# Optimization experiments

Hardware: AMD Instinct MI355X
Metric: run time of the kernel (lower is better)

The kernel has to match this reference:

```python
import jax, jax.numpy as jnp
import numpy as np

H, W, DIM, NB = 64, 128, 768, 8
BS = DIM // NB
LAM = 0.01  # sparsity_threshold
EPS = 1e-5


def _layernorm(x, g, b):
    mu = jnp.mean(x, axis=-1, keepdims=True)
    var = jnp.mean(jnp.square(x - mu), axis=-1, keepdims=True)
    return (x - mu) * jax.lax.rsqrt(var + EPS) * g + b


def _softshrink(v):
    return jnp.sign(v) * jnp.maximum(jnp.abs(v) - LAM, 0.0)


def setup_inputs() -> dict:
    key = jax.random.key(0)
    ks = jax.random.split(key, 6)
    B = 4
    x = jax.random.normal(ks[0], (B, H * W, DIM), dtype=jnp.float32)
    w1 = 0.02 * jax.random.normal(ks[1], (NB, BS, BS), dtype=jnp.float32)
    b1 = 0.02 * jax.random.normal(ks[2], (NB, BS), dtype=jnp.float32)
    w2 = 0.02 * jax.random.normal(ks[3], (NB, BS, BS), dtype=jnp.float32)
    b2 = 0.02 * jax.random.normal(ks[4], (NB, BS), dtype=jnp.float32)
    km = jax.random.split(ks[5], 2)
    mlp_w1 = (1.0 / np.sqrt(DIM)) * jax.random.normal(km[0], (DIM, 4 * DIM), dtype=jnp.float32)
    mlp_w2 = (1.0 / np.sqrt(4 * DIM)) * jax.random.normal(km[1], (4 * DIM, DIM), dtype=jnp.float32)
    return {
        'x': x, 'w1': w1, 'b1': b1, 'w2': w2, 'b2': b2,
        'ln1_w': jnp.ones((DIM,), jnp.float32), 'ln1_b': jnp.zeros((DIM,), jnp.float32),
        'ln2_w': jnp.ones((DIM,), jnp.float32), 'ln2_b': jnp.zeros((DIM,), jnp.float32),
        'mlp_w1': mlp_w1, 'mlp_b1': jnp.zeros((4 * DIM,), jnp.float32),
        'mlp_w2': mlp_w2, 'mlp_b2': jnp.zeros((DIM,), jnp.float32),
    }


def reference(x, w1, b1, w2, b2, ln1_w, ln1_b, ln2_w, ln2_b, mlp_w1, mlp_b1, mlp_w2, mlp_b2):
    B = x.shape[0]
    xs = x.reshape(B, H, W, DIM)
    residual = xs
    xn = _layernorm(xs, ln1_w, ln1_b)
    xn = jnp.transpose(xn, (0, 3, 1, 2))  # [B, dim, h, w]
    xf = jnp.fft.rfft2(xn, norm='ortho')  # [B, dim, h, w//2+1] complex64
    Wf = xf.shape[-1]
    xf = xf.reshape(B, NB, BS, H, Wf)
    xr, xi = xf.real, xf.imag

    def bmm(t, Wm):  # block-diagonal matmul over feature dim j->m
        return jnp.einsum('bnjkl,njm->bnmkl', t, Wm)

    bb1 = b1[None, :, :, None, None]
    bb2 = b2[None, :, :, None, None]
    # NOTE: faithful to source -- both real and imag paths use the SAME weight matrix.
    o1r = jax.nn.relu(bmm(xr, w1) - bmm(xi, w1) + bb1)
    o1i = jax.nn.relu(bmm(xi, w1) + bmm(xr, w1) + bb1)
    o2r = bmm(o1r, w2) - bmm(o1i, w2) + bb2
    o2i = bmm(o1i, w2) + bmm(o1r, w2) + bb2
    o2 = _softshrink(o2r) + 1j * _softshrink(o2i)
    o2 = o2.reshape(B, DIM, H, Wf)
    xsp = jnp.fft.irfft2(o2, s=(H, W), norm='ortho')  # [B, dim, h, w]
    xsp = jnp.transpose(xsp, (0, 2, 3, 1)) + residual
    residual2 = xsp
    xn2 = _layernorm(xsp, ln2_w, ln2_b)
    hdd = jax.nn.gelu(xn2 @ mlp_w1 + mlp_b1, approximate=False)
    out = hdd @ mlp_w2 + mlp_b2 + residual2
    return out.reshape(B, H * W, DIM)
```

## Files before the change

kernel.cpp:

```cpp
#include <hip/hip_runtime.h>
#include <hip/hip_bf16.h>
#include <math.h>

#define B_    4
#define H_    64
#define W_    128
#define WF_   65
#define D_    768
#define NB_   8
#define BS_   96
#define HID_  3072
#define NTOK_ 32768
#define CHTOK_ 8192
#define LAM_  0.01f

typedef __hip_bfloat16 bf16;
typedef __attribute__((ext_vector_type(8))) short bf16x8;
typedef __attribute__((ext_vector_type(4))) float f32x4;
typedef unsigned int u32;

__device__ __forceinline__ float ldf(const float* p) { return *p; }
__device__ __forceinline__ float ldf(const bf16* p)  { return __bfloat162float(*p); }
__device__ __forceinline__ void stf(float* p, float v) { *p = v; }
__device__ __forceinline__ void stf(bf16* p, float v)  { *p = __float2bfloat16(v); }

#define GLOAD_LDS16(g, l) \
  __builtin_amdgcn_global_load_lds((const __attribute__((address_space(1))) u32*)(g), \
                                   (__attribute__((address_space(3))) u32*)(l), 16, 0, 0)

#define FRAG(arr, KP, row, kof) (*(const bf16x8*)((arr) + (size_t)(row) * (KP) + (kof)))

#define LUT_S1_OFF  0
#define LUT_S2M_OFF 22528
#define LUT_S2P_OFF 36864
#define LUT_S3_OFF  51200
#define LUT_TOTAL   77824

__global__ __launch_bounds__(256) void lut_init(bf16* __restrict__ lut) {
  const int idx = blockIdx.x * 256 + threadIdx.x;
  const float s1 = 0.011048543456039806f;
  float val = 0.f;
  if (idx < 22528) {
    int a = idx;
    if (a < 21760) {
      bool isC2 = a >= 10880; if (isC2) a -= 10880;
      int f = a / 136, w = a - f * 136;
      if (w < 128) {
        int p = (f * w) & 127;
        float ang = p * 0.04908738521234052f;
        val = isC2 ? -s1 * sinf(ang) : s1 * cosf(ang);
      }
    }
  } else if (idx < 51200) {
    int a = idx - 22528;
    float esign = -1.f;
    if (a >= 14336) { a -= 14336; esign = 1.f; }
    if (a < 13824) {
      int which = a / 4608; a -= which * 4608;
      int k = a / 72, h = a - k * 72;
      if (h < 64) {
        int p = (k * h) & 63;
        float ang = p * 0.09817477042468103f;
        float c = cosf(ang), s = esign * sinf(ang);
        val = (which == 0) ? c : ((which == 1) ? s : -s);
      }
    }
  } else {
    int a = idx - 51200;
    bool isCi = a >= 13312; if (isCi) a -= 13312;
    int w = a / 104, f = a - w * 104;
    if (f < WF_) {
      int p = (f * w) & 127;
      float ang = p * 0.04908738521234052f;
      float al = (f == 0 || f == 64) ? 1.0f : 2.0f;
      val = isCi ? -s1 * al * sinf(ang) : s1 * al * cosf(ang);
    }
  }
  lut[idx] = __float2bfloat16(val);
}

template <typename TIN>
__global__ __launch_bounds__(256) void ln_kernel(
    const TIN* __restrict__ x, const float* __restrict__ g,
    const float* __restrict__ bta, bf16* __restrict__ out) {
  __shared__ float sred[8];
  const size_t base = (size_t)blockIdx.x * D_;
  const int t = threadIdx.x;
  float v0 = ldf(x + base + t);
  float v1 = ldf(x + base + t + 256);
  float v2 = ldf(x + base + t + 512);
  float s = v0 + v1 + v2;
  #pragma unroll
  for (int o = 32; o; o >>= 1) s += __shfl_down(s, o, 64);
  int lane = t & 63, wid = t >> 6;
  if (lane == 0) sred[wid] = s;
  __syncthreads();
  if (t == 0) sred[0] = sred[0] + sred[1] + sred[2] + sred[3];
  __syncthreads();
  float mean = sred[0] * (1.0f / D_);
  float d0 = v0 - mean, d1 = v1 - mean, d2 = v2 - mean;
  float q = d0 * d0 + d1 * d1 + d2 * d2;
  #pragma unroll
  for (int o = 32; o; o >>= 1) q += __shfl_down(q, o, 64);
  if (lane == 0) sred[4 + wid] = q;
  __syncthreads();
  if (t == 0) sred[4] = sred[4] + sred[5] + sred[6] + sred[7];
  __syncthreads();
  float rstd = rsqrtf(sred[4] * (1.0f / D_) + 1e-5f);
  stf(out + base + t,       d0 * rstd * g[t]       + bta[t]);
  stf(out + base + t + 256, d1 * rstd * g[t + 256] + bta[t + 256]);
  stf(out + base + t + 512, d2 * rstd * g[t + 512] + bta[t + 512]);
}

__global__ __launch_bounds__(256) void s1_rfftw(
    const bf16* __restrict__ xn, const bf16* __restrict__ lut,
    bf16* __restrict__ fr, bf16* __restrict__ fi) {
  const int KP = 136;
  __shared__ __align__(16) bf16 sC[22528];
  __shared__ __align__(16) bf16 sXt[64 * 136];
  const int t = threadIdx.x;
  const int bh = blockIdx.x;
  const int c0 = blockIdx.y * 64;

  #pragma unroll
  for (int it = 0; it < 11; ++it)
    GLOAD_LDS16((const char*)lut + t * 16 + it * 4096, (char*)sC + t * 16 + it * 4096);

  {
    const int cv = (t & 7) * 8;
    #pragma unroll
    for (int rep = 0; rep < 4; ++rep) {
      int w = (t >> 3) + 32 * rep;
      bf16x8 v = *(const bf16x8*)(xn + ((size_t)bh * W_ + w) * D_ + c0 + cv);
      #pragma unroll
      for (int i = 0; i < 8; ++i) sXt[(cv + i) * KP + w] = ((const bf16*)&v)[i];
    }
  }
  __syncthreads();
  const bf16* sC1 = sC;
  const bf16* sC2 = sC + 10880;

  const int wave = t >> 6, lane = t & 63, l16 = lane & 15, quad = lane >> 4;
  const int ni = (wave == 0) ? 2 : 1;
  int itile[2] = {wave, 4};
  f32x4 accR[2][4], accI[2][4];
  #pragma unroll
  for (int ii = 0; ii < 2; ++ii)
    #pragma unroll
    for (int j = 0; j < 4; ++j) { accR[ii][j] = (f32x4){0,0,0,0}; accI[ii][j] = (f32x4){0,0,0,0}; }

  for (int s = 0; s < 4; ++s) {
    const int kof = s * 32 + quad * 8;
    bf16x8 bfrag[4];
    #pragma unroll
    for (int j = 0; j < 4; ++j) bfrag[j] = FRAG(sXt, KP, j * 16 + l16, kof);
    for (int ii = 0; ii < ni; ++ii) {
      const int arow = 16 * itile[ii] + l16;
      bf16x8 a1 = FRAG(sC1, KP, arow, kof);
      bf16x8 a2 = FRAG(sC2, KP, arow, kof);
      #pragma unroll
      for (int j = 0; j < 4; ++j) {
        accR[ii][j] = __builtin_amdgcn_mfma_f32_16x16x32_bf16(a1, bfrag[j], accR[ii][j], 0, 0, 0);
        accI[ii][j] = __builtin_amdgcn_mfma_f32_16x16x32_bf16(a2, bfrag[j], accI[ii][j], 0, 0, 0);
      }
    }
  }
  for (int ii = 0; ii < ni; ++ii) {
    #pragma unroll
    for (int r = 0; r < 4; ++r) {
      const int f = 16 * itile[ii] + quad * 4 + r;
      if (f >= WF_) continue;
      const size_t ob = ((size_t)bh * WF_ + f) * D_ + c0;
      #pragma unroll
      for (int j = 0; j < 4; ++j) {
        fr[ob + j * 16 + l16] = __float2bfloat16(accR[ii][j][r]);
        fi[ob + j * 16 + l16] = __float2bfloat16(accI[ii][j][r]);
      }
    }
  }
}

__global__ __launch_bounds__(256) void s2_ffth(
    const bf16* __restrict__ inr, const bf16* __restrict__ ini,
    bf16* __restrict__ outr, bf16* __restrict__ outi, const bf16* __restrict__ lut) {
  const int KP = 72;
  __shared__ __align__(16) bf16 sT[14336];
  __shared__ __align__(16) bf16 sFtr[64 * 72];
  __shared__ __align__(16) bf16 sFti[64 * 72];
  const int t = threadIdx.x;
  const int b = blockIdx.x / WF_;
  const int f = blockIdx.x % WF_;
  const int c0 = blockIdx.y * 64;

  #pragma unroll
  for (int it = 0; it < 7; ++it)
    GLOAD_LDS16((const char*)lut + t * 16 + it * 4096, (char*)sT + t * 16 + it * 4096);

  {
    const int cv = (t & 7) * 8;
    #pragma unroll
    for (int rep = 0; rep < 2; ++rep) {
      int h = (t >> 3) + 32 * rep;
      size_t g = ((size_t)(b * H_ + h) * WF_ + f) * D_ + c0 + cv;
      bf16x8 vr = *(const bf16x8*)(inr + g);
      bf16x8 vi = *(const bf16x8*)(ini + g);
      #pragma unroll
      for (int i = 0; i < 8; ++i) {
        sFtr[(cv + i) * KP + h] = ((const bf16*)&vr)[i];
        sFti[(cv + i) * KP + h] = ((const bf16*)&vi)[i];
      }
    }
  }
  __syncthreads();
  const bf16* sTr = sT;
  const bf16* sTi = sT + 4608;
  const bf16* sTn = sT + 9216;

  const int wave = t >> 6, lane = t & 63, l16 = lane & 15, quad = lane >> 4;
  f32x4 accR[4], accI[4];
  #pragma unroll
  for (int j = 0; j < 4; ++j) { accR[j] = (f32x4){0,0,0,0}; accI[j] = (f32x4){0,0,0,0}; }

  #pragma unroll
  for (int s = 0; s < 2; ++s) {
    const int kof = s * 32 + quad * 8;
    const int arow = 16 * wave + l16;
    bf16x8 ar = FRAG(sTr, KP, arow, kof);
    bf16x8 ai = FRAG(sTi, KP, arow, kof);
    bf16x8 an = FRAG(sTn, KP, arow, kof);
    #pragma unroll
    for (int j = 0; j < 4; ++j) {
      const int brow = j * 16 + l16;
      bf16x8 br = FRAG(sFtr, KP, brow, kof);
      bf16x8 bi = FRAG(sFti, KP, brow, kof);
      accR[j] = __builtin_amdgcn_mfma_f32_16x16x32_bf16(ar, br, accR[j], 0, 0, 0);
      accR[j] = __builtin_amdgcn_mfma_f32_16x16x32_bf16(an, bi, accR[j], 0, 0, 0);
      accI[j] = __builtin_amdgcn_mfma_f32_16x16x32_bf16(ai, br, accI[j], 0, 0, 0);
      accI[j] = __builtin_amdgcn_mfma_f32_16x16x32_bf16(ar, bi, accI[j], 0, 0, 0);
    }
  }
  #pragma unroll
  for (int r = 0; r < 4; ++r) {
    const int k = 16 * wave + quad * 4 + r;
    const size_t ob = ((size_t)(b * H_ + k) * WF_ + f) * D_ + c0;
    #pragma unroll
    for (int j = 0; j < 4; ++j) {
      outr[ob + j * 16 + l16] = __float2bfloat16(accR[j][r]);
      outi[ob + j * 16 + l16] = __float2bfloat16(accI[j][r]);
    }
  }
}

__global__ __launch_bounds__(256) void s3_irfftw(
    const bf16* __restrict__ fr, const bf16* __restrict__ fi,
    const bf16* __restrict__ lut, const float* __restrict__ x0, bf16* __restrict__ xsp) {
  const int KP = 104;
  __shared__ __align__(16) bf16 sC[26624];
  __shared__ __align__(16) bf16 sGtr[64 * 104];
  __shared__ __align__(16) bf16 sGti[64 * 104];
  const int t = threadIdx.x;
  const int bh = blockIdx.x;
  const int c0 = blockIdx.y * 64;

  #pragma unroll
  for (int it = 0; it < 13; ++it)
    GLOAD_LDS16((const char*)lut + t * 16 + it * 4096, (char*)sC + t * 16 + it * 4096);

  {
    const int cv = (t & 7) * 8;
    #pragma unroll
    for (int rep = 0; rep < 2; ++rep) {
      int f = (t >> 3) + 32 * rep;
      size_t g = ((size_t)bh * WF_ + f) * D_ + c0 + cv;
      bf16x8 vr = *(const bf16x8*)(fr + g);
      bf16x8 vi = *(const bf16x8*)(fi + g);
      #pragma unroll
      for (int i = 0; i < 8; ++i) {
        sGtr[(cv + i) * KP + f] = ((const bf16*)&vr)[i];
        sGti[(cv + i) * KP + f] = ((const bf16*)&vi)[i];
      }
    }
    if (t < 8) {
      size_t g = ((size_t)bh * WF_ + 64) * D_ + c0 + cv;
      bf16x8 vr = *(const bf16x8*)(fr + g);
      bf16x8 vi = *(const bf16x8*)(fi + g);
      #pragma unroll
      for (int i = 0; i < 8; ++i) {
        sGtr[(cv + i) * KP + 64] = ((const bf16*)&vr)[i];
        sGti[(cv + i) * KP + 64] = ((const bf16*)&vi)[i];
      }
    }
    const bf16 z = __float2bfloat16(0.f);
    for (int e = t; e < 64 * 31; e += 256) {
      int c = e / 31, f = 65 + (e - (e / 31) * 31);
      sGtr[c * KP + f] = z;
      sGti[c * KP + f] = z;
    }
  }
  __syncthreads();
  const bf16* sCr = sC;
  const bf16* sCi = sC + 13312;

  const int wave = t >> 6, lane = t & 63, l16 = lane & 15, quad = lane >> 4;
  f32x4 acc[2][4];
  #pragma unroll
  for (int ii = 0; ii < 2; ++ii)
    #pragma unroll
    for (int j = 0; j < 4; ++j) acc[ii][j] = (f32x4){0,0,0,0};

  #pragma unroll
  for (int s = 0; s < 3; ++s) {
    const int kof = s * 32 + quad * 8;
    bf16x8 br[4], bi[4];
    #pragma unroll
    for (int j = 0; j < 4; ++j) {
      br[j] = FRAG(sGtr, KP, j * 16 + l16, kof);
      bi[j] = FRAG(sGti, KP, j * 16 + l16, kof);
    }
    #pragma unroll
    for (int ii = 0; ii < 2; ++ii) {
      const int arow = 16 * (wave + 4 * ii) + l16;
      bf16x8 a1 = FRAG(sCr, KP, arow, kof);
      bf16x8 a2 = FRAG(sCi, KP, arow, kof);
      #pragma unroll
      for (int j = 0; j < 4; ++j) {
        acc[ii][j] = __builtin_amdgcn_mfma_f32_16x16x32_bf16(a1, br[j], acc[ii][j], 0, 0, 0);
        acc[ii][j] = __builtin_amdgcn_mfma_f32_16x16x32_bf16(a2, bi[j], acc[ii][j], 0, 0, 0);
      }
    }
  }
  #pragma unroll
  for (int ii = 0; ii < 2; ++ii) {
    #pragma unroll
    for (int r = 0; r < 4; ++r) {
      const int w = 16 * (wave + 4 * ii) + quad * 4 + r;
      const size_t ob = ((size_t)bh * W_ + w) * D_ + c0;
      #pragma unroll
      for (int j = 0; j < 4; ++j) {
        const size_t o = ob + j * 16 + l16;
        xsp[o] = __float2bfloat16(acc[ii][j][r] + x0[o]);
      }
    }
  }
}

__global__ __launch_bounds__(256) void blockmlp_mfma(
    bf16* __restrict__ gr, bf16* __restrict__ gi,
    const float* __restrict__ w1, const float* __restrict__ b1,
    const float* __restrict__ w2, const float* __restrict__ b2) {
  const int KP = 104;
  __shared__ __align__(16) bf16 sA[128 * 104];
  __shared__ __align__(16) bf16 sW[96 * 104];
  const int t = threadIdx.x;
  const int p0 = blockIdx.x * 64;
  const int nb = blockIdx.y;
  const int cbase = nb * BS_;

  #pragma unroll
  for (int it = 0; it < 3; ++it) {
    int task = t + 256 * it;
    int r = task / 12, jv = task - r * 12;
    size_t g = (size_t)(p0 + r) * D_ + cbase + jv * 8;
    bf16x8 vr = *(const bf16x8*)(gr + g);
    bf16x8 vi = *(const bf16x8*)(gi + g);
    bf16x8 u8, v8;
    #pragma unroll
    for (int i = 0; i < 8; ++i) {
      float xr = __bfloat162float(((const bf16*)&vr)[i]);
      float xi = __bfloat162float(((const bf16*)&vi)[i]);
      ((bf16*)&u8)[i] = __float2bfloat16(xr - xi);
      ((bf16*)&v8)[i] = __float2bfloat16(xr + xi);
    }
    *(bf16x8*)(sA + r * KP + jv * 8) = u8;
    *(bf16x8*)(sA + (64 + r) * KP + jv * 8) = v8;
  }
  {
    const float* wsrc = w1 + nb * BS_ * BS_;
    #pragma unroll
    for (int it = 0; it < 9; ++it) {
      int e4 = t + 256 * it;
      int j = e4 / 24, m4 = (e4 - j * 24) * 4;
      float4 ld = *(const float4*)(wsrc + j * 96 + m4);
      sW[(m4 + 0) * KP + j] = __float2bfloat16(ld.x);
      sW[(m4 + 1) * KP + j] = __float2bfloat16(ld.y);
      sW[(m4 + 2) * KP + j] = __float2bfloat16(ld.z);
      sW[(m4 + 3) * KP + j] = __float2bfloat16(ld.w);
    }
  }
  __syncthreads();

  const int wave = t >> 6, lane = t & 63, l16 = lane & 15, quad = lane >> 4;
  f32x4 accU[6], accV[6];
  #pragma unroll
  for (int n = 0; n < 6; ++n) { accU[n] = (f32x4){0,0,0,0}; accV[n] = (f32x4){0,0,0,0}; }

  #pragma unroll
  for (int s = 0; s < 3; ++s) {
    const int kof = s * 32 + quad * 8;
    bf16x8 au = FRAG(sA, KP, wave * 16 + l16, kof);
    bf16x8 av = FRAG(sA, KP, 64 + wave * 16 + l16, kof);
    bf16x8 bw[6];
    #pragma unroll
    for (int n = 0; n < 6; ++n) bw[n] = FRAG(sW, KP, n * 16 + l16, kof);
    #pragma unroll
    for (int n = 0; n < 6; ++n) {
      accU[n] = __builtin_amdgcn_mfma_f32_16x16x32_bf16(au, bw[n], accU[n], 0, 0, 0);
      accV[n] = __builtin_amdgcn_mfma_f32_16x16x32_bf16(av, bw[n], accV[n], 0, 0, 0);
    }
  }
  __syncthreads();

  {
    const float* wsrc = w2 + nb * BS_ * BS_;
    #pragma unroll
    for (int it = 0; it < 9; ++it) {
      int e4 = t + 256 * it;
      int j = e4 / 24, m4 = (e4 - j * 24) * 4;
      float4 ld = *(const float4*)(wsrc + j * 96 + m4);
      sW[(m4 + 0) * KP + j] = __float2bfloat16(ld.x);
      sW[(m4 + 1) * KP + j] = __float2bfloat16(ld.y);
      sW[(m4 + 2) * KP + j] = __float2bfloat16(ld.z);
      sW[(m4 + 3) * KP + j] = __float2bfloat16(ld.w);
    }
  }
  #pragma unroll
  for (int n = 0; n < 6; ++n) {
    const float bias = b1[cbase + n * 16 + l16];
    #pragma unroll
    for (int r = 0; r < 4; ++r) {
      float o1r = fmaxf(accU[n][r] + bias, 0.0f);
      float o1i = fmaxf(accV[n][r] + bias, 0.0f);
      const int row = wave * 16 + quad * 4 + r;
      sA[row * KP + n * 16 + l16]        = __float2bfloat16(o1r - o1i);
      sA[(64 + row) * KP + n * 16 + l16] = __float2bfloat16(o1r + o1i);
    }
  }
  __syncthreads();

  #pragma unroll
  for (int n = 0; n < 6; ++n) { accU[n] = (f32x4){0,0,0,0}; accV[n] = (f32x4){0,0,0,0}; }
  #pragma unroll
  for (int s = 0; s < 3; ++s) {
    const int kof = s * 32 + quad * 8;
    bf16x8 ap = FRAG(sA, KP, wave * 16 + l16, kof);
    bf16x8 aq = FRAG(sA, KP, 64 + wave * 16 + l16, kof);
    bf16x8 bw[6];
    #pragma unroll
    for (int n = 0; n < 6; ++n) bw[n] = FRAG(sW, KP, n * 16 + l16, kof);
    #pragma unroll
    for (int n = 0; n < 6; ++n) {
      accU[n] = __builtin_amdgcn_mfma_f32_16x16x32_bf16(ap, bw[n], accU[n], 0, 0, 0);
      accV[n] = __builtin_amdgcn_mfma_f32_16x16x32_bf16(aq, bw[n], accV[n], 0, 0, 0);
    }
  }

  #pragma unroll
  for (int n = 0; n < 6; ++n) {
    const float bias = b2[cbase + n * 16 + l16];
    #pragma unroll
    for (int r = 0; r < 4; ++r) {
      const int row = wave * 16 + quad * 4 + r;
      float o2r = accU[n][r] + bias;
      float o2i = accV[n][r] + bias;
      o2r = (o2r > LAM_) ? (o2r - LAM_) : ((o2r < -LAM_) ? (o2r + LAM_) : 0.0f);
      o2i = (o2i > LAM_) ? (o2i - LAM_) : ((o2i < -LAM_) ? (o2i + LAM_) : 0.0f);
      const size_t o = (size_t)(p0 + row) * D_ + cbase + n * 16 + l16;
      gr[o] = __float2bfloat16(o2r);
      gi[o] = __float2bfloat16(o2i);
    }
  }
}

__global__ __launch_bounds__(256) void wtrans_kernel(
    const float* __restrict__ Wm, bf16* __restrict__ Wt, int K, int N) {
  __shared__ float tile[32][33];
  const int n0 = blockIdx.x * 32;
  const int k0 = blockIdx.y * 32;
  const int tx = threadIdx.x & 31;
  const int ty = threadIdx.x >> 5;
  #pragma unroll
  for (int r = 0; r < 32; r += 8)
    tile[ty + r][tx] = Wm[(size_t)(k0 + ty + r) * N + n0 + tx];
  __syncthreads();
  #pragma unroll
  for (int r = 0; r < 32; r += 8)
    Wt[(size_t)(n0 + ty + r) * K + k0 + tx] = __float2bfloat16(tile[tx][ty + r]);
}

template <int MODE, typename TOUT>
__global__ __launch_bounds__(256) void mfma_gemm_kernel(
    const bf16* __restrict__ A, const bf16* __restrict__ Bt,
    const float* __restrict__ bias, const bf16* __restrict__ resid,
    TOUT* __restrict__ out, int M, int N, int K) {
  __shared__ __align__(16) bf16 As[2][128 * 32];
  __shared__ __align__(16) bf16 Bs[2][128 * 32];
  const int t = threadIdx.x;
  const int m0 = blockIdx.x * 128;
  const int n0 = blockIdx.y * 128;
  const int wave = t >> 6;
  const int lane = t & 63;
  const int wm = (wave & 1) * 64;
  const int wn = (wave >> 1) * 64;
  const int l16 = lane & 15;
  const int quad = lane >> 4;

  const int srow = t >> 2;
  const int skof = ((t & 3) ^ ((srow >> 1) & 3)) * 8;
  const bf16* Ag0 = A + (size_t)(m0 + srow) * K + skof;
  const bf16* Ag1 = A + (size_t)(m0 + 64 + srow) * K + skof;
  const bf16* Bg0 = Bt + (size_t)(n0 + srow) * K + skof;
  const bf16* Bg1 = Bt + (size_t)(n0 + 64 + srow) * K + skof;

  int aoff[4], boff[4];
  #pragma unroll
  for (int i = 0; i < 4; ++i) {
    const int ra = wm + i * 16 + l16;
    aoff[i] = ra * 32 + (quad ^ ((ra >> 1) & 3)) * 8;
    const int rb = wn + i * 16 + l16;
    boff[i] = rb * 32 + (quad ^ ((rb >> 1) & 3)) * 8;
  }

  f32x4 acc[4][4];
  #pragma unroll
  for (int i = 0; i < 4; ++i)
    #pragma unroll
    for (int j = 0; j < 4; ++j) acc[i][j] = (f32x4){0.f, 0.f, 0.f, 0.f};

#define STAGE_G(bb, ko) do { \
    GLOAD_LDS16(Ag0 + (ko), &As[bb][t * 8]); \
    GLOAD_LDS16(Ag1 + (ko), &As[bb][2048 + t * 8]); \
    GLOAD_LDS16(Bg0 + (ko), &Bs[bb][t * 8]); \
    GLOAD_LDS16(Bg1 + (ko), &Bs[bb][2048 + t * 8]); } while (0)

#define COMPUTE_T(bb) do { \
    bf16x8 af[4], bfr[4]; \
    _Pragma("unroll") \
    for (int i = 0; i < 4; ++i) af[i] = *(const bf16x8*)(As[bb] + aoff[i]); \
    _Pragma("unroll") \
    for (int j = 0; j < 4; ++j) bfr[j] = *(const bf16x8*)(Bs[bb] + boff[j]); \
    _Pragma("unroll") \
    for (int i = 0; i < 4; ++i) \
      _Pragma("unroll") \
      for (int j = 0; j < 4; ++j) \
        acc[i][j] = __builtin_amdgcn_mfma_f32_16x16x32_bf16(af[i], bfr[j], acc[i][j], 0, 0, 0); \
  } while (0)

  const int NT = K >> 5;
  STAGE_G(0, 0);
  asm volatile("s_waitcnt vmcnt(0)" ::: "memory");
  __builtin_amdgcn_s_barrier();
  asm volatile("" ::: "memory");
  int cur = 0;
  for (int tt = 0; tt + 1 < NT; ++tt) {
    STAGE_G(cur ^ 1, (tt + 1) << 5);
    COMPUTE_T(cur);
    asm volatile("s_waitcnt vmcnt(0)" ::: "memory");
    __builtin_amdgcn_s_barrier();
    asm volatile("" ::: "memory");
    cur ^= 1;
  }
  COMPUTE_T(cur);
#undef STAGE_G
#undef COMPUTE_T

  #pragma unroll
  for (int i = 0; i < 4; ++i) {
    #pragma unroll
    for (int j = 0; j < 4; ++j) {
      const int n = n0 + wn + j * 16 + l16;
      const float bz = bias[n];
      #pragma unroll
      for (int r = 0; r < 4; ++r) {
        const int m = m0 + wm + i * 16 + quad * 4 + r;
        float v = acc[i][j][r] + bz;
        if (MODE == 0) {
          float q = v * fmaf(0.044715f, v * v, 1.0f);
          float e = __expf(-1.5957691216f * q);
          v = v * __builtin_amdgcn_rcpf(1.0f + e);
        } else {
          v += ldf(resid + (size_t)m * N + n);
        }
        stf(out + (size_t)m * N + n, v);
      }
    }
  }
}

extern "C" void kernel_launch(void* const* d_in, const int* in_sizes, int n_in,
                              void* d_out, int out_size, void* d_ws, size_t ws_size,
                              hipStream_t stream) {
  const float* x     = (const float*)d_in[0];
  const float* w1    = (const float*)d_in[1];
  const float* b1    = (const float*)d_in[2];
  const float* w2    = (const float*)d_in[3];
  const float* b2    = (const float*)d_in[4];
  const float* ln1w  = (const float*)d_in[5];
  const float* ln1b  = (const float*)d_in[6];
  const float* ln2w  = (const float*)d_in[7];
  const float* ln2b  = (const float*)d_in[8];
  const float* mlpw1 = (const float*)d_in[9];
  const float* mlpb1 = (const float*)d_in[10];
  const float* mlpw2 = (const float*)d_in[11];
  const float* mlpb2 = (const float*)d_in[12];
  float* out = (float*)d_out;

  const size_t SPA = (size_t)B_ * H_ * W_ * D_;
  const size_t FRE = (size_t)B_ * H_ * WF_ * D_;
  bf16* ws   = (bf16*)d_ws;
  bf16* bufA = ws;
  bf16* Fr   = bufA + SPA;
  bf16* Fi   = Fr + FRE;
  bf16* Gr   = Fi + FRE;
  bf16* Gi   = Gr + FRE;
  bf16* hid  = Fr;
  bf16* xn2c = Gr;
  bf16* w1t  = xn2c + (size_t)CHTOK_ * D_;
  bf16* w2t  = w1t + (size_t)D_ * HID_;

  bf16* lut = (bf16*)d_out;

  const int nspec = B_ * H_ * WF_;

  hipLaunchKernelGGL(lut_init, dim3(LUT_TOTAL / 256), dim3(256), 0, stream, lut);
  hipLaunchKernelGGL((ln_kernel<float>), dim3(NTOK_), dim3(256), 0, stream, x, ln1w, ln1b, bufA);
  hipLaunchKernelGGL(s1_rfftw, dim3(B_ * H_, D_ / 64), dim3(256), 0, stream,
                     bufA, lut + LUT_S1_OFF, Fr, Fi);
  hipLaunchKernelGGL(s2_ffth, dim3(B_ * WF_, D_ / 64), dim3(256), 0, stream,
                     Fr, Fi, Gr, Gi, lut + LUT_S2M_OFF);
  hipLaunchKernelGGL(blockmlp_mfma, dim3(nspec / 64, NB_), dim3(256), 0, stream,
                     Gr, Gi, w1, b1, w2, b2);
  hipLaunchKernelGGL(s2_ffth, dim3(B_ * WF_, D_ / 64), dim3(256), 0, stream,
                     Gr, Gi, Fr, Fi, lut + LUT_S2P_OFF);
  hipLaunchKernelGGL(s3_irfftw, dim3(B_ * H_, D_ / 64), dim3(256), 0, stream,
                     Fr, Fi, lut + LUT_S3_OFF, x, bufA);

  hipLaunchKernelGGL(wtrans_kernel, dim3(HID_ / 32, D_ / 32), dim3(256), 0, stream,
                     mlpw1, w1t, D_, HID_);
  hipLaunchKernelGGL(wtrans_kernel, dim3(D_ / 32, HID_ / 32), dim3(256), 0, stream,
                     mlpw2, w2t, HID_, D_);

  for (int c = 0; c < B_; ++c) {
    const bf16* rs = bufA + (size_t)c * CHTOK_ * D_;
    float* oc = out + (size_t)c * CHTOK_ * D_;
    hipLaunchKernelGGL((ln_kernel<bf16>), dim3(CHTOK_), dim3(256), 0, stream,
                       rs, ln2w, ln2b, xn2c);
    hipLaunchKernelGGL((mfma_gemm_kernel<0, bf16>), dim3(CHTOK_ / 128, HID_ / 128), dim3(256), 0,
                       stream, xn2c, w1t, mlpb1, (const bf16*)nullptr, hid, CHTOK_, HID_, D_);
    hipLaunchKernelGGL((mfma_gemm_kernel<1, float>), dim3(CHTOK_ / 128, D_ / 128), dim3(256), 0,
                       stream, hid, w2t, mlpb2, rs, oc, CHTOK_, D_, HID_);
  }
}
```

Measured before the change: 945.3 us.

## Triple-buffer MFMA GEMM LDS staging with partial vmcnt waits and setprio

```diff
diff --git a/kernel.cpp b/kernel.cpp
--- a/kernel.cpp
+++ b/kernel.cpp
@@ -492,8 +492,8 @@
     const bf16* __restrict__ A, const bf16* __restrict__ Bt,
     const float* __restrict__ bias, const bf16* __restrict__ resid,
     TOUT* __restrict__ out, int M, int N, int K) {
-  __shared__ __align__(16) bf16 As[2][128 * 32];
-  __shared__ __align__(16) bf16 Bs[2][128 * 32];
+  __shared__ __align__(16) bf16 As[3][128 * 32];
+  __shared__ __align__(16) bf16 Bs[3][128 * 32];
   const int t = threadIdx.x;
   const int m0 = blockIdx.x * 128;
   const int n0 = blockIdx.y * 128;
@@ -538,30 +538,37 @@
     for (int i = 0; i < 4; ++i) af[i] = *(const bf16x8*)(As[bb] + aoff[i]); \
     _Pragma("unroll") \
     for (int j = 0; j < 4; ++j) bfr[j] = *(const bf16x8*)(Bs[bb] + boff[j]); \
+    __builtin_amdgcn_s_setprio(1); \
     _Pragma("unroll") \
     for (int i = 0; i < 4; ++i) \
       _Pragma("unroll") \
       for (int j = 0; j < 4; ++j) \
         acc[i][j] = __builtin_amdgcn_mfma_f32_16x16x32_bf16(af[i], bfr[j], acc[i][j], 0, 0, 0); \
+    __builtin_amdgcn_s_setprio(0); \
   } while (0)
+
+#define WAITBAR(n) do { \
+    asm volatile("s_waitcnt vmcnt(" #n ")" ::: "memory"); \
+    __builtin_amdgcn_s_barrier(); \
+    asm volatile("" ::: "memory"); } while (0)
 
   const int NT = K >> 5;
   STAGE_G(0, 0);
-  asm volatile("s_waitcnt vmcnt(0)" ::: "memory");
-  __builtin_amdgcn_s_barrier();
-  asm volatile("" ::: "memory");
-  int cur = 0;
-  for (int tt = 0; tt + 1 < NT; ++tt) {
-    STAGE_G(cur ^ 1, (tt + 1) << 5);
-    COMPUTE_T(cur);
-    asm volatile("s_waitcnt vmcnt(0)" ::: "memory");
-    __builtin_amdgcn_s_barrier();
-    asm volatile("" ::: "memory");
-    cur ^= 1;
-  }
-  COMPUTE_T(cur);
+  STAGE_G(1, 32);
+  WAITBAR(4);
+  int bcur = 0, bnxt = 1, bstg = 2;
+  for (int tt = 0; tt < NT - 2; ++tt) {
+    STAGE_G(bstg, (tt + 2) << 5);
+    COMPUTE_T(bcur);
+    WAITBAR(4);
+    int tmp = bcur; bcur = bnxt; bnxt = bstg; bstg = tmp;
+  }
+  COMPUTE_T(bcur);
+  WAITBAR(0);
+  COMPUTE_T(bnxt);
 #undef STAGE_G
 #undef COMPUTE_T
+#undef WAITBAR
 
   #pragma unroll
   for (int i = 0; i < 4; ++i) {
```

Measured after the change: 924.2 us. 2.2% less time.

## Enlarge MLP GEMM tile to 128x256 with 8 waves and triple-buffered K=64 stages

Applied to the files above, without the earlier changes.

```diff
diff --git a/kernel.cpp b/kernel.cpp
--- a/kernel.cpp
+++ b/kernel.cpp
@@ -488,37 +488,33 @@
 }
 
 template <int MODE, typename TOUT>
-__global__ __launch_bounds__(256) void mfma_gemm_kernel(
+__global__ __launch_bounds__(512) void mfma_gemm_kernel(
     const bf16* __restrict__ A, const bf16* __restrict__ Bt,
     const float* __restrict__ bias, const bf16* __restrict__ resid,
     TOUT* __restrict__ out, int M, int N, int K) {
-  __shared__ __align__(16) bf16 As[2][128 * 32];
-  __shared__ __align__(16) bf16 Bs[2][128 * 32];
+  __shared__ __align__(16) bf16 sM[3 * 24576];
   const int t = threadIdx.x;
   const int m0 = blockIdx.x * 128;
-  const int n0 = blockIdx.y * 128;
-  const int wave = t >> 6;
-  const int lane = t & 63;
-  const int wm = (wave & 1) * 64;
-  const int wn = (wave >> 1) * 64;
-  const int l16 = lane & 15;
-  const int quad = lane >> 4;
-
-  const int srow = t >> 2;
-  const int skof = ((t & 3) ^ ((srow >> 1) & 3)) * 8;
-  const bf16* Ag0 = A + (size_t)(m0 + srow) * K + skof;
-  const bf16* Ag1 = A + (size_t)(m0 + 64 + srow) * K + skof;
-  const bf16* Bg0 = Bt + (size_t)(n0 + srow) * K + skof;
-  const bf16* Bg1 = Bt + (size_t)(n0 + 64 + srow) * K + skof;
-
-  int aoff[4], boff[4];
-  #pragma unroll
-  for (int i = 0; i < 4; ++i) {
-    const int ra = wm + i * 16 + l16;
-    aoff[i] = ra * 32 + (quad ^ ((ra >> 1) & 3)) * 8;
-    const int rb = wn + i * 16 + l16;
-    boff[i] = rb * 32 + (quad ^ ((rb >> 1) & 3)) * 8;
-  }
+  const int n0 = blockIdx.y * 256;
+  const int wave = t >> 6, lane = t & 63, l16 = lane & 15, quad = lane >> 4;
+  const int wr = wave >> 2, wc = wave & 3;
+
+  const int srow = t >> 3;
+  const int scol = ((t & 7) ^ (srow & 7)) * 8;
+  const bf16* Ag0 = A + (size_t)(m0 + srow) * K + scol;
+  const bf16* Ag1 = A + (size_t)(m0 + 64 + srow) * K + scol;
+  const bf16* Bg0 = Bt + (size_t)(n0 + srow) * K + scol;
+  const bf16* Bg1 = Bt + (size_t)(n0 + 64 + srow) * K + scol;
+  const bf16* Bg2 = Bt + (size_t)(n0 + 128 + srow) * K + scol;
+  const bf16* Bg3 = Bt + (size_t)(n0 + 192 + srow) * K + scol;
+
+  int arow[4], brow[4], sofs[2];
+  #pragma unroll
+  for (int i = 0; i < 4; ++i) arow[i] = (wr * 64 + i * 16 + l16) * 64;
+  #pragma unroll
+  for (int j = 0; j < 4; ++j) brow[j] = 8192 + (wc * 64 + j * 16 + l16) * 64;
+  sofs[0] = (quad ^ (l16 & 7)) * 8;
+  sofs[1] = ((4 + quad) ^ (l16 & 7)) * 8;
 
   f32x4 acc[4][4];
   #pragma unroll
@@ -526,52 +522,63 @@
     #pragma unroll
     for (int j = 0; j < 4; ++j) acc[i][j] = (f32x4){0.f, 0.f, 0.f, 0.f};
 
-#define STAGE_G(bb, ko) do { \
-    GLOAD_LDS16(Ag0 + (ko), &As[bb][t * 8]); \
-    GLOAD_LDS16(Ag1 + (ko), &As[bb][2048 + t * 8]); \
-    GLOAD_LDS16(Bg0 + (ko), &Bs[bb][t * 8]); \
-    GLOAD_LDS16(Bg1 + (ko), &Bs[bb][2048 + t * 8]); } while (0)
-
-#define COMPUTE_T(bb) do { \
+#define STAGE6(bb, ko) do { \
+    bf16* d_ = sM + (bb) * 24576; \
+    GLOAD_LDS16(Ag0 + (ko), d_ + t * 8); \
+    GLOAD_LDS16(Ag1 + (ko), d_ + 4096 + t * 8); \
+    GLOAD_LDS16(Bg0 + (ko), d_ + 8192 + t * 8); \
+    GLOAD_LDS16(Bg1 + (ko), d_ + 12288 + t * 8); \
+    GLOAD_LDS16(Bg2 + (ko), d_ + 16384 + t * 8); \
+    GLOAD_LDS16(Bg3 + (ko), d_ + 20480 + t * 8); } while (0)
+
+#define PHASE(bb, s) do { \
+    const bf16* base_ = sM + (bb) * 24576; \
     bf16x8 af[4], bfr[4]; \
     _Pragma("unroll") \
-    for (int i = 0; i < 4; ++i) af[i] = *(const bf16x8*)(As[bb] + aoff[i]); \
+    for (int i = 0; i < 4; ++i) af[i] = *(const bf16x8*)(base_ + arow[i] + sofs[s]); \
     _Pragma("unroll") \
-    for (int j = 0; j < 4; ++j) bfr[j] = *(const bf16x8*)(Bs[bb] + boff[j]); \
+    for (int j = 0; j < 4; ++j) bfr[j] = *(const bf16x8*)(base_ + brow[j] + sofs[s]); \
+    __builtin_amdgcn_s_setprio(1); \
     _Pragma("unroll") \
     for (int i = 0; i < 4; ++i) \
       _Pragma("unroll") \
       for (int j = 0; j < 4; ++j) \
         acc[i][j] = __builtin_amdgcn_mfma_f32_16x16x32_bf16(af[i], bfr[j], acc[i][j], 0, 0, 0); \
+    __builtin_amdgcn_s_setprio(0); \
   } while (0)
 
-  const int NT = K >> 5;
-  STAGE_G(0, 0);
-  asm volatile("s_waitcnt vmcnt(0)" ::: "memory");
+  const int NT = K >> 6;
+  STAGE6(0, 0);
+  STAGE6(1, 64);
+  asm volatile("s_waitcnt vmcnt(6)" ::: "memory");
   __builtin_amdgcn_s_barrier();
   asm volatile("" ::: "memory");
+
   int cur = 0;
-  for (int tt = 0; tt + 1 < NT; ++tt) {
-    STAGE_G(cur ^ 1, (tt + 1) << 5);
-    COMPUTE_T(cur);
-    asm volatile("s_waitcnt vmcnt(0)" ::: "memory");
+  for (int kt = 0; kt < NT; ++kt) {
+    int stg = cur + 2; if (stg >= 3) stg -= 3;
+    const bool more = (kt + 2 < NT);
+    if (more) STAGE6(stg, (size_t)(kt + 2) << 6);
+    PHASE(cur, 0);
+    PHASE(cur, 1);
+    if (more) { asm volatile("s_waitcnt vmcnt(6)" ::: "memory"); }
+    else      { asm volatile("s_waitcnt vmcnt(0)" ::: "memory"); }
     __builtin_amdgcn_s_barrier();
     asm volatile("" ::: "memory");
-    cur ^= 1;
-  }
-  COMPUTE_T(cur);
-#undef STAGE_G
-#undef COMPUTE_T
+    ++cur; if (cur == 3) cur = 0;
+  }
+#undef STAGE6
+#undef PHASE
 
   #pragma unroll
   for (int i = 0; i < 4; ++i) {
     #pragma unroll
     for (int j = 0; j < 4; ++j) {
-      const int n = n0 + wn + j * 16 + l16;
+      const int n = n0 + wc * 64 + j * 16 + l16;
       const float bz = bias[n];
       #pragma unroll
       for (int r = 0; r < 4; ++r) {
-        const int m = m0 + wm + i * 16 + quad * 4 + r;
+        const int m = m0 + wr * 64 + i * 16 + quad * 4 + r;
         float v = acc[i][j][r] + bz;
         if (MODE == 0) {
           float q = v * fmaf(0.044715f, v * v, 1.0f);
@@ -644,9 +651,9 @@
     float* oc = out + (size_t)c * CHTOK_ * D_;
     hipLaunchKernelGGL((ln_kernel<bf16>), dim3(CHTOK_), dim3(256), 0, stream,
                        rs, ln2w, ln2b, xn2c);
-    hipLaunchKernelGGL((mfma_gemm_kernel<0, bf16>), dim3(CHTOK_ / 128, HID_ / 128), dim3(256), 0,
+    hipLaunchKernelGGL((mfma_gemm_kernel<0, bf16>), dim3(CHTOK_ / 128, HID_ / 256), dim3(512), 0,
                        stream, xn2c, w1t, mlpb1, (const bf16*)nullptr, hid, CHTOK_, HID_, D_);
-    hipLaunchKernelGGL((mfma_gemm_kernel<1, float>), dim3(CHTOK_ / 128, D_ / 128), dim3(256), 0,
+    hipLaunchKernelGGL((mfma_gemm_kernel<1, float>), dim3(CHTOK_ / 128, D_ / 256), dim3(512), 0,
                        stream, hid, w2t, mlpb2, rs, oc, CHTOK_, D_, HID_);
   }
 }
```

After: 837.7 us. 11.4% less time.
